# Performance work log

Measured on AMD Instinct MI355X. Metric: run time of the kernel, lower is better.

Reference implementation:

```python
import jax, jax.numpy as jnp
import numpy as np

D = 256; NH = 8; NL = 4; NP = 4; HD = D // NH
SHAPES = np.array([[180, 180], [90, 90], [45, 45], [23, 23]], dtype=np.int32)
LQ = int((SHAPES[:, 0] * SHAPES[:, 1]).sum())  # 43054
STARTS = np.concatenate([[0], np.cumsum(SHAPES[:, 0] * SHAPES[:, 1])[:-1]]).astype(np.int32)


def setup_inputs():
    ks = jax.random.split(jax.random.key(0), 16)
    s = 0.02
    p = lambda k, shp: jax.random.normal(k, shp, jnp.float32) * s
    return {
        "query": jax.random.normal(ks[0], (1, LQ, D), jnp.float32),
        "ref_points": jax.random.uniform(ks[1], (1, LQ, NL, 2), dtype=jnp.float32),
        "pos": jax.random.normal(ks[2], (1, LQ, D), jnp.float32),
        "input_spatial_shapes": jnp.asarray(SHAPES),
        "input_level_start_index": jnp.asarray(STARTS),
        "w_off": p(ks[3], (D, NH * NL * NP * 2)), "b_off": p(ks[4], (NH * NL * NP * 2,)),
        "w_attn": p(ks[5], (D, NH * NL * NP)), "b_attn": p(ks[6], (NH * NL * NP,)),
        "w_val": p(ks[7], (D, D)), "b_val": jnp.zeros((D,), jnp.float32),
        "w_out": p(ks[8], (D, D)), "b_out": jnp.zeros((D,), jnp.float32),
        "g1": jnp.ones((D,), jnp.float32), "beta1": jnp.zeros((D,), jnp.float32),
        "w1": p(ks[9], (D, D)), "b1": jnp.zeros((D,), jnp.float32),
        "w2": p(ks[10], (D, D)), "b2": jnp.zeros((D,), jnp.float32),
        "g2": jnp.ones((D,), jnp.float32), "beta2": jnp.zeros((D,), jnp.float32),
    }


def _ln(x, g, b):
    m = x.mean(-1, keepdims=True)
    v = ((x - m) ** 2).mean(-1, keepdims=True)
    return (x - m) * jax.lax.rsqrt(v + 1e-5) * g + b


def _sample_level(v, Hl, Wl, loc):
    # v: (B, Hl*Wl, NH, HD); loc: (B, Lq, NH, NP, 2) normalized to [0,1]
    # Bilinear sampling matching F.grid_sample(align_corners=False, padding_mode='zeros')
    B, _, nh, d = v.shape
    Lq, P = loc.shape[1], loc.shape[3]
    vb = jnp.transpose(v, (0, 2, 1, 3))  # (B, NH, HW, d)
    x = loc[..., 0] * Wl - 0.5
    y = loc[..., 1] * Hl - 0.5
    x0 = jnp.floor(x); y0 = jnp.floor(y)
    fx = x - x0; fy = y - y0
    out = jnp.zeros((B, nh, Lq, P, d), v.dtype)
    for dy in (0, 1):
        for dx in (0, 1):
            xi = x0 + dx; yi = y0 + dy
            w = (fx if dx else 1.0 - fx) * (fy if dy else 1.0 - fy)
            valid = (xi >= 0) & (xi < Wl) & (yi >= 0) & (yi < Hl)
            xc = jnp.clip(xi, 0, Wl - 1).astype(jnp.int32)
            yc = jnp.clip(yi, 0, Hl - 1).astype(jnp.int32)
            idx = jnp.transpose(yc * Wl + xc, (0, 2, 1, 3)).reshape(B, nh, Lq * P)
            g = jnp.take_along_axis(vb, idx[..., None], axis=2).reshape(B, nh, Lq, P, d)
            wt = jnp.transpose(jnp.where(valid, w, 0.0), (0, 2, 1, 3))
            out = out + g * wt[..., None]
    return out  # (B, NH, Lq, NP, HD)


def _layer(query, ref_points, pos, shp, sti, w_off, b_off, w_attn, b_attn, w_val, b_val,
           w_out, b_out, g1, beta1, w1, b1, w2, b2, g2, beta2):
    B, Lq, _ = query.shape
    q = query + pos  # with_pos_embed
    value = (query @ w_val + b_val).reshape(B, Lq, NH, HD)
    off = (q @ w_off + b_off).reshape(B, Lq, NH, NL, NP, 2)
    aw = jax.nn.softmax((q @ w_attn + b_attn).reshape(B, Lq, NH, NL * NP), axis=-1)
    aw = aw.reshape(B, Lq, NH, NL, NP)
    # offset_normalizer = [W_l, H_l]
    norm = jnp.asarray(shp[:, ::-1].copy(), jnp.float32)
    loc = ref_points[:, :, None, :, None, :] + off / norm[None, None, None, :, None, :]
    acc = jnp.zeros((B, NH, Lq, HD), query.dtype)
    for l in range(NL):
        Hl, Wl = int(shp[l, 0]), int(shp[l, 1])
        st = int(sti[l])
        sampled = _sample_level(value[:, st:st + Hl * Wl], Hl, Wl, loc[:, :, :, l])
        wl = jnp.transpose(aw[:, :, :, l], (0, 2, 1, 3))  # (B, NH, Lq, NP)
        acc = acc + (sampled * wl[..., None]).sum(axis=3)
    attn_out = acc.transpose(0, 2, 1, 3).reshape(B, Lq, D) @ w_out + b_out
    # residual + LayerNorm + FFN (dropout is identity in eval mode)
    x = _ln(query + attn_out, g1, beta1)
    ffn = jax.nn.relu(x @ w1 + b1) @ w2 + b2
    return _ln(x + ffn, g2, beta2)


def reference(query, ref_points, pos, input_spatial_shapes, input_level_start_index,
              w_off, b_off, w_attn, b_attn, w_val, b_val, w_out, b_out,
              g1, beta1, w1, b1, w2, b2, g2, beta2):
    shp = np.asarray(input_spatial_shapes)
    sti = np.asarray(input_level_start_index)
    return _layer(query, ref_points, pos, shp, sti, w_off, b_off, w_attn, b_attn,
                  w_val, b_val, w_out, b_out, g1, beta1, w1, b1, w2, b2, g2, beta2)
```

## Files before the change

kernel.cpp:

```cpp
#include <hip/hip_runtime.h>

typedef unsigned short u16;
typedef unsigned int u32;
typedef float f32x4 __attribute__((ext_vector_type(4)));
typedef short i16x8 __attribute__((ext_vector_type(8)));
typedef __bf16 bf16x8_t __attribute__((ext_vector_type(8)));

#define LQ 43054

__device__ __forceinline__ float bf2f(u16 u) {
  union { u32 i; float f; } v; v.i = ((u32)u) << 16; return v.f;
}
__device__ __forceinline__ u16 f2bf(float f) {
  u32 i = __float_as_uint(f);
  return (u16)((i + 0x7FFFu + ((i >> 16) & 1u)) >> 16);
}

__device__ __forceinline__ float dot2bf(u32 v, u32 w, float c) {
  float d;
  asm("v_dot2_f32_bf16 %0, %1, %2, %3" : "=v"(d) : "v"(v), "v"(w), "v"(c));
  return d;
}

template <typename T>
__device__ __forceinline__ auto mfma_try(T a, T b, f32x4 c, int)
    -> decltype(__builtin_amdgcn_mfma_f32_16x16x32_bf16(a, b, c, 0, 0, 0)) {
  return __builtin_amdgcn_mfma_f32_16x16x32_bf16(a, b, c, 0, 0, 0);
}
template <typename T>
__device__ __forceinline__ f32x4 mfma_try(T a, T b, f32x4 c, long) {
  return __builtin_amdgcn_mfma_f32_16x16x32_bf16(
      __builtin_bit_cast(bf16x8_t, a), __builtin_bit_cast(bf16x8_t, b), c, 0, 0, 0);
}
__device__ __forceinline__ f32x4 mfma_bf16(i16x8 a, i16x8 b, f32x4 c) {
  return mfma_try(a, b, c, 0);
}

__global__ void transpose_all_kernel(
    const float* __restrict__ w_off, const float* __restrict__ w_attn,
    const float* __restrict__ w_val, const float* __restrict__ w_out,
    const float* __restrict__ w1, const float* __restrict__ w2,
    u16* __restrict__ wT) {
  int b = blockIdx.x;
  const float* src; u16* dst; int N; int col;
  if (b < 256)       { src = w_off;  dst = wT;          N = 256; col = b; }
  else if (b < 384)  { src = w_attn; dst = wT + 65536;  N = 128; col = b - 256; }
  else if (b < 640)  { src = w_val;  dst = wT + 98304;  N = 256; col = b - 384; }
  else if (b < 896)  { src = w_out;  dst = wT + 163840; N = 256; col = b - 640; }
  else if (b < 1152) { src = w1;     dst = wT + 229376; N = 256; col = b - 896; }
  else               { src = w2;     dst = wT + 294912; N = 256; col = b - 1152; }
  dst[col * 256 + threadIdx.x] = f2bf(src[threadIdx.x * N + col]);
}

__device__ __forceinline__ void stage_a_dma(uint4* As, const u16* A, int r0, int M,
                                            int w, int lane) {
#pragma unroll
  for (int jj = 0; jj < 8; ++jj) {
    int row = w * 16 + jj * 2 + (lane >> 5);
    int gr = min(r0 + row, M - 1);
    int c = lane & 31;
    const uint4* gp = (const uint4*)A + (size_t)gr * 32 + (c ^ (row & 7));
    __builtin_amdgcn_global_load_lds(
        (const __attribute__((address_space(1))) void*)gp,
        (__attribute__((address_space(3))) void*)(As + (w * 16 + jj * 2) * 32),
        16, 0, 0);
  }
}
template <int ADD, int PH>
__device__ __forceinline__ void stage_a_f32(uint4* As, const float* A, const float* A2,
                                            int r0, int M, int tid) {
  constexpr int IT = 16 / PH;
#pragma unroll
  for (int h = 0; h < PH; ++h) {
    float4 va[IT];
    float4 vp[ADD ? IT : 1];
#pragma unroll
    for (int it = 0; it < IT; ++it) {
      int e = tid + (h * IT + it) * 256;
      int gr = min(r0 + (e >> 6), M - 1);
      int idx = gr * 64 + (e & 63);
      va[it] = ((const float4*)A)[idx];
      if constexpr (ADD) vp[it] = ((const float4*)A2)[idx];
    }
#pragma unroll
    for (int it = 0; it < IT; ++it) {
      int e = tid + (h * IT + it) * 256;
      int row = e >> 6, c4 = e & 63;
      float4 v = va[it];
      if constexpr (ADD) {
        v.x += vp[it].x; v.y += vp[it].y; v.z += vp[it].z; v.w += vp[it].w;
      }
      uint2 pk;
      pk.x = (u32)f2bf(v.x) | ((u32)f2bf(v.y) << 16);
      pk.y = (u32)f2bf(v.z) | ((u32)f2bf(v.w) << 16);
      int c = c4 >> 1, hf = c4 & 1;
      ((uint2*)As)[((row * 32 + (c ^ (row & 7))) << 1) | hf] = pk;
    }
  }
}
__device__ __forceinline__ void load_b(i16x8* f, const u16* Bt, int t, int l16, int quad) {
  const uint4* bp = (const uint4*)Bt + (t * 16 + l16) * 32 + quad;
#pragma unroll
  for (int kk = 0; kk < 8; ++kk) f[kk] = __builtin_bit_cast(i16x8, bp[kk << 2]);
}
__device__ __forceinline__ void tile_mfma(f32x4* acc, const uint4* As,
                                          const i16x8* bfr, int l16, int quad) {
#pragma unroll
  for (int rg = 0; rg < 4; ++rg) {
    int arow = rg * 16 + l16;
    f32x4 a = {0.f, 0.f, 0.f, 0.f};
#pragma unroll
    for (int kk = 0; kk < 8; ++kk) {
      i16x8 afr = __builtin_bit_cast(i16x8, As[arow * 32 + (((kk << 2) + quad) ^ (arow & 7))]);
      a = mfma_bf16(afr, bfr[kk], a);
    }
    acc[rg] = a;
  }
}

__device__ __forceinline__ int swz_u16(int row, int col) {
  return row * 256 + ((((col >> 3) ^ (row & 7)) << 3) | (col & 7));
}

#define LS_STRIDE 264
__device__ __forceinline__ void lds_store_rows(const u16* Ls, u16* out,
                                               int r0, int M, int w, int lane) {
#pragma unroll
  for (int it = 0; it < 8; ++it) {
    int lrow = w * 16 + it * 2 + (lane >> 5);
    int grow = r0 + lrow;
    int chunk = lane & 31;
    if (grow < M) {
      *(uint4*)(out + (size_t)grow * 256 + chunk * 8) =
          *(const uint4*)(Ls + lrow * LS_STRIDE + chunk * 8);
    }
  }
}

template <int AIN, int MODE>
__global__ __launch_bounds__(256, 3) void gemm_kernel(
    const void* __restrict__ Av, const u16* __restrict__ Bt,
    const float* __restrict__ bias, void* __restrict__ out, int M) {
  __shared__ uint4 As[2176];
  const int tid = threadIdx.x;
  const int w = tid >> 6, lane = tid & 63, quad = lane >> 4, l16 = lane & 15;
  const int r0 = blockIdx.x * 64;
  if constexpr (AIN == 2) stage_a_dma(As, (const u16*)Av, r0, M, w, lane);
  else                    stage_a_f32<0, 2>(As, (const float*)Av, nullptr, r0, M, tid);
  __syncthreads();
  i16x8 bfr[2][8];
  load_b(bfr[0], Bt, w * 4, l16, quad);
  f32x4 vals[4][4];
#pragma unroll
  for (int i = 0; i < 4; ++i) {
    const int t = w * 4 + i;
    if (i + 1 < 4) load_b(bfr[(i + 1) & 1], Bt, t + 1, l16, quad);
    tile_mfma(vals[i], As, bfr[i & 1], l16, quad);
  }
  __syncthreads();
  u16* Ls = (u16*)As;
#pragma unroll
  for (int i = 0; i < 4; ++i) {
    const int col = (w * 4 + i) * 16 + l16;
    const float bv = bias[col];
#pragma unroll
    for (int rg = 0; rg < 4; ++rg)
#pragma unroll
      for (int r = 0; r < 4; ++r) {
        float v = vals[i][rg][r] + bv;
        if (MODE == 2) v = fmaxf(v, 0.f);
        Ls[(rg * 16 + (quad << 2) + r) * LS_STRIDE + col] = f2bf(v);
      }
  }
  __syncthreads();
  lds_store_rows(Ls, (u16*)out, r0, M, w, lane);
}

__global__ __launch_bounds__(256, 3) void offaw_gemm_kernel(
    const float* __restrict__ query, const float* __restrict__ pos,
    const u16* __restrict__ Bt, const float* __restrict__ b_off,
    const float* __restrict__ b_attn, u16* __restrict__ offb,
    float* __restrict__ aw, int M) {
  __shared__ uint4 As[2176];
  const int tid = threadIdx.x;
  const int w = tid >> 6, lane = tid & 63, quad = lane >> 4, l16 = lane & 15;
  const int r0 = blockIdx.x * 64;
  stage_a_f32<1, 4>(As, query, pos, r0, M, tid);
  __syncthreads();
  i16x8 bfr[2][8];
  load_b(bfr[0], Bt, w, l16, quad);
  f32x4 vals[4][4];
#pragma unroll
  for (int i = 0; i < 6; ++i) {
    const int t = w + 4 * i;
    if (i + 1 < 6) load_b(bfr[(i + 1) & 1], Bt, w + 4 * (i + 1), l16, quad);
    if (i < 4) {
      tile_mfma(vals[i], As, bfr[i & 1], l16, quad);
    } else {
      f32x4 acc[4];
      tile_mfma(acc, As, bfr[i & 1], l16, quad);
      const int colc = (t - 16) * 16 + l16;
      const float bv = b_attn[colc];
#pragma unroll
      for (int rg = 0; rg < 4; ++rg)
#pragma unroll
        for (int r = 0; r < 4; ++r) {
          float v = acc[rg][r] + bv;
          float m = v;
#pragma unroll
          for (int o = 1; o < 16; o <<= 1) m = fmaxf(m, __shfl_xor(m, o));
          float e = __expf(v - m);
          float s = e;
#pragma unroll
          for (int o = 1; o < 16; o <<= 1) s += __shfl_xor(s, o);
          int row = r0 + rg * 16 + (quad << 2) + r;
          if (row < M) aw[row * 128 + colc] = e / s;
        }
    }
  }
  __syncthreads();
  u16* Ls = (u16*)As;
#pragma unroll
  for (int i = 0; i < 4; ++i) {
    const int col = (w + 4 * i) * 16 + l16;
    const float bv = b_off[col];
#pragma unroll
    for (int rg = 0; rg < 4; ++rg)
#pragma unroll
      for (int r = 0; r < 4; ++r)
        Ls[(rg * 16 + (quad << 2) + r) * LS_STRIDE + col] = f2bf(vals[i][rg][r] + bv);
  }
  __syncthreads();
  lds_store_rows(Ls, offb, r0, M, w, lane);
}

__global__ __launch_bounds__(256, 2) void tail_fused_kernel(
    const u16* __restrict__ accb, const u16* __restrict__ woutT,
    const float* __restrict__ b_out, const float* __restrict__ query,
    const float* __restrict__ g1, const float* __restrict__ beta1,
    const u16* __restrict__ w1T, const float* __restrict__ b1,
    const u16* __restrict__ w2T, const float* __restrict__ b2,
    const float* __restrict__ g2, const float* __restrict__ beta2,
    float* __restrict__ out, int M) {
  __shared__ uint4 As[2048];
  __shared__ uint4 Xs[2048];
  __shared__ float2 pnorm[256];
  const int tid = threadIdx.x;
  const int w = tid >> 6, lane = tid & 63, quad = lane >> 4, l16 = lane & 15;
  const int r0 = blockIdx.x * 64;
  stage_a_dma(As, accb, r0, M, w, lane);
  __syncthreads();
  i16x8 bfr[2][8];
  f32x4 vals[4][4];
  float s[16], s2[16];

  load_b(bfr[0], woutT, w * 4, l16, quad);
#pragma unroll
  for (int i = 0; i < 4; ++i) {
    if (i + 1 < 4) load_b(bfr[(i + 1) & 1], woutT, w * 4 + i + 1, l16, quad);
    tile_mfma(vals[i], As, bfr[i & 1], l16, quad);
  }
#pragma unroll
  for (int k = 0; k < 16; ++k) { s[k] = 0.f; s2[k] = 0.f; }
#pragma unroll
  for (int i = 0; i < 4; ++i) {
    const int col = (w * 4 + i) * 16 + l16;
    const float bv = b_out[col];
#pragma unroll
    for (int rg = 0; rg < 4; ++rg)
#pragma unroll
      for (int r = 0; r < 4; ++r) {
        int row = r0 + rg * 16 + (quad << 2) + r;
        float rv = (row < M) ? query[row * 256 + col] : 0.f;
        float v = vals[i][rg][r] + bv + rv;
        vals[i][rg][r] = v;
        s[rg * 4 + r] += v; s2[rg * 4 + r] += v * v;
      }
  }
#pragma unroll
  for (int k = 0; k < 16; ++k)
#pragma unroll
    for (int o = 1; o < 16; o <<= 1) {
      s[k] += __shfl_xor(s[k], o);
      s2[k] += __shfl_xor(s2[k], o);
    }
  if (l16 == 0) {
#pragma unroll
    for (int rg = 0; rg < 4; ++rg)
#pragma unroll
      for (int r = 0; r < 4; ++r)
        pnorm[(rg * 16 + (quad << 2) + r) * 4 + w] = make_float2(s[rg * 4 + r], s2[rg * 4 + r]);
  }
  __syncthreads();
  u16* Xu = (u16*)Xs;
#pragma unroll
  for (int rg = 0; rg < 4; ++rg)
#pragma unroll
    for (int r = 0; r < 4; ++r) {
      int lrow = rg * 16 + (quad << 2) + r;
      float4 p01 = ((const float4*)pnorm)[lrow * 2];
      float4 p23 = ((const float4*)pnorm)[lrow * 2 + 1];
      float ss = p01.x + p01.z + p23.x + p23.z;
      float qq = p01.y + p01.w + p23.y + p23.w;
      float mean = ss * (1.f / 256.f);
      float var = qq * (1.f / 256.f) - mean * mean;
      float inv = rsqrtf(var + 1e-5f);
#pragma unroll
      for (int i = 0; i < 4; ++i) {
        const int col = (w * 4 + i) * 16 + l16;
        float o = (vals[i][rg][r] - mean) * inv * g1[col] + beta1[col];
        Xu[swz_u16(lrow, col)] = f2bf(o);
      }
    }
  __syncthreads();

  load_b(bfr[0], w1T, w * 4, l16, quad);
#pragma unroll
  for (int i = 0; i < 4; ++i) {
    if (i + 1 < 4) load_b(bfr[(i + 1) & 1], w1T, w * 4 + i + 1, l16, quad);
    tile_mfma(vals[i], Xs, bfr[i & 1], l16, quad);
  }
  u16* Hu = (u16*)As;
#pragma unroll
  for (int i = 0; i < 4; ++i) {
    const int col = (w * 4 + i) * 16 + l16;
    const float bv = b1[col];
#pragma unroll
    for (int rg = 0; rg < 4; ++rg)
#pragma unroll
      for (int r = 0; r < 4; ++r) {
        int lrow = rg * 16 + (quad << 2) + r;
        Hu[swz_u16(lrow, col)] = f2bf(fmaxf(vals[i][rg][r] + bv, 0.f));
      }
  }
  __syncthreads();

  load_b(bfr[0], w2T, w * 4, l16, quad);
#pragma unroll
  for (int i = 0; i < 4; ++i) {
    if (i + 1 < 4) load_b(bfr[(i + 1) & 1], w2T, w * 4 + i + 1, l16, quad);
    tile_mfma(vals[i], As, bfr[i & 1], l16, quad);
  }
#pragma unroll
  for (int k = 0; k < 16; ++k) { s[k] = 0.f; s2[k] = 0.f; }
#pragma unroll
  for (int i = 0; i < 4; ++i) {
    const int col = (w * 4 + i) * 16 + l16;
    const float bv = b2[col];
#pragma unroll
    for (int rg = 0; rg < 4; ++rg)
#pragma unroll
      for (int r = 0; r < 4; ++r) {
        int lrow = rg * 16 + (quad << 2) + r;
        float xv = bf2f(Xu[swz_u16(lrow, col)]);
        float v = vals[i][rg][r] + bv + xv;
        vals[i][rg][r] = v;
        s[rg * 4 + r] += v; s2[rg * 4 + r] += v * v;
      }
  }
#pragma unroll
  for (int k = 0; k < 16; ++k)
#pragma unroll
    for (int o = 1; o < 16; o <<= 1) {
      s[k] += __shfl_xor(s[k], o);
      s2[k] += __shfl_xor(s2[k], o);
    }
  if (l16 == 0) {
#pragma unroll
    for (int rg = 0; rg < 4; ++rg)
#pragma unroll
      for (int r = 0; r < 4; ++r)
        pnorm[(rg * 16 + (quad << 2) + r) * 4 + w] = make_float2(s[rg * 4 + r], s2[rg * 4 + r]);
  }
  __syncthreads();
#pragma unroll
  for (int rg = 0; rg < 4; ++rg)
#pragma unroll
    for (int r = 0; r < 4; ++r) {
      int lrow = rg * 16 + (quad << 2) + r;
      float4 p01 = ((const float4*)pnorm)[lrow * 2];
      float4 p23 = ((const float4*)pnorm)[lrow * 2 + 1];
      float ss = p01.x + p01.z + p23.x + p23.z;
      float qq = p01.y + p01.w + p23.y + p23.w;
      float mean = ss * (1.f / 256.f);
      float var = qq * (1.f / 256.f) - mean * mean;
      float inv = rsqrtf(var + 1e-5f);
      int row = r0 + lrow;
      if (row < M) {
#pragma unroll
        for (int i = 0; i < 4; ++i) {
          const int col = (w * 4 + i) * 16 + l16;
          out[row * 256 + col] = (vals[i][rg][r] - mean) * inv * g2[col] + beta2[col];
        }
      }
    }
}

__global__ __launch_bounds__(256) void sampler_kernel(
    const float* __restrict__ refp, const u16* __restrict__ offb,
    const float* __restrict__ aw, const u16* __restrict__ value,
    u32* __restrict__ accv) {
  __shared__ uint4 rec[544];
  const int t = threadIdx.x;
  const int nwg = gridDim.x;
  const int qd = nwg >> 3, rm = nwg & 7;
  const int xcd = blockIdx.x & 7, ii = blockIdx.x >> 3;
  const int b = (xcd < rm ? xcd * (qd + 1) : rm * (qd + 1) + (xcd - rm) * qd) + ii;
#pragma unroll
  for (int it = 0; it < 2; ++it) {
    const int sidx = t + it * 256;
    const int qs = sidx >> 7, j = sidx & 127;
    const int i = b * 4 + qs;
    if (i < LQ) {
      const int h = j >> 4, lp = j & 15, l = lp >> 2;
      const int Wl = (l == 0) ? 180 : (l == 1) ? 90 : (l == 2) ? 45 : 23;
      const int st = (l == 0) ? 0 : (l == 1) ? 32400 : (l == 2) ? 40500 : 42525;
      const float wj = aw[i * 128 + j];
      const u32 o2 = *(const u32*)(offb + i * 256 + h * 32 + lp * 2);
      const float ox = bf2f((u16)(o2 & 0xffffu)), oy = bf2f((u16)(o2 >> 16));
      const float rx = refp[i * 8 + l * 2], ry = refp[i * 8 + l * 2 + 1];
      float x = rx * (float)Wl + ox - 0.5f;
      float y = ry * (float)Wl + oy - 0.5f;
      float x0f = floorf(x), y0f = floorf(y);
      float fx = x - x0f, fy = y - y0f;
      int x0 = (int)x0f, y0 = (int)y0f;
      bool vx0 = (x0 >= 0) & (x0 < Wl), vx1 = (x0 + 1 >= 0) & (x0 + 1 < Wl);
      bool vy0 = (y0 >= 0) & (y0 < Wl), vy1 = (y0 + 1 >= 0) & (y0 + 1 < Wl);
      int x0c = min(max(x0, 0), Wl - 1), x1c = min(max(x0 + 1, 0), Wl - 1);
      int y0c = min(max(y0, 0), Wl - 1), y1c = min(max(y0 + 1, 0), Wl - 1);
      float w00 = (vx0 & vy0) ? wj * (1.f - fx) * (1.f - fy) : 0.f;
      float w01 = (vx1 & vy0) ? wj * fx * (1.f - fy) : 0.f;
      float w10 = (vx0 & vy1) ? wj * (1.f - fx) * fy : 0.f;
      float w11 = (vx1 & vy1) ? wj * fx * fy : 0.f;
      uint4 r;
      r.x = (u32)((st + y0c * Wl + x0c) * 512 + h * 64) | (u32)(x1c - x0c);
      r.y = (u32)(y1c - y0c) * (u32)(Wl * 512);
      r.z = (u32)f2bf(w00) | ((u32)f2bf(w01) << 16);
      r.w = (u32)f2bf(w10) | ((u32)f2bf(w11) << 16);
      rec[qs * 136 + h * 17 + lp] = r;
    }
  }
  __syncthreads();
  const int qs = t >> 6, j2 = t & 63;
  const int h = j2 >> 3, dp8 = j2 & 7;
  const int i = b * 4 + qs;
  if (i >= LQ) return;
  const char* vb = (const char*)value;
  float a0 = 0.f, a1 = 0.f, a2 = 0.f, a3 = 0.f;
  const int rbase = qs * 136 + h * 17;
  const u32 dpo = (u32)(dp8 * 8);
#pragma unroll
  for (int p = 0; p < 16; ++p) {
    uint4 r = rec[rbase + p];
    u32 base = (r.x & 0xFFFFFFFEu) + dpo;
    u32 dxo = (r.x & 1u) << 9;
    u32 dyo = r.y;
    uint2 p00 = *(const uint2*)(vb + base);
    uint2 p01 = *(const uint2*)(vb + base + dxo);
    uint2 p10 = *(const uint2*)(vb + base + dyo);
    uint2 p11 = *(const uint2*)(vb + base + dyo + dxo);
    a0 = dot2bf(__builtin_amdgcn_perm(p01.x, p00.x, 0x05040100u), r.z, a0);
    a1 = dot2bf(__builtin_amdgcn_perm(p01.x, p00.x, 0x07060302u), r.z, a1);
    a2 = dot2bf(__builtin_amdgcn_perm(p01.y, p00.y, 0x05040100u), r.z, a2);
    a3 = dot2bf(__builtin_amdgcn_perm(p01.y, p00.y, 0x07060302u), r.z, a3);
    a0 = dot2bf(__builtin_amdgcn_perm(p11.x, p10.x, 0x05040100u), r.w, a0);
    a1 = dot2bf(__builtin_amdgcn_perm(p11.x, p10.x, 0x07060302u), r.w, a1);
    a2 = dot2bf(__builtin_amdgcn_perm(p11.y, p10.y, 0x05040100u), r.w, a2);
    a3 = dot2bf(__builtin_amdgcn_perm(p11.y, p10.y, 0x07060302u), r.w, a3);
  }
  uint2 pk;
  pk.x = (u32)f2bf(a0) | ((u32)f2bf(a1) << 16);
  pk.y = (u32)f2bf(a2) | ((u32)f2bf(a3) << 16);
  ((uint2*)accv)[i * 64 + h * 8 + dp8] = pk;
}

extern "C" void kernel_launch(void* const* d_in, const int* in_sizes, int n_in,
                              void* d_out, int out_size, void* d_ws, size_t ws_size,
                              hipStream_t stream) {
  const float* query  = (const float*)d_in[0];
  const float* refp   = (const float*)d_in[1];
  const float* pos    = (const float*)d_in[2];
  const float* w_off  = (const float*)d_in[5];
  const float* b_off  = (const float*)d_in[6];
  const float* w_attn = (const float*)d_in[7];
  const float* b_attn = (const float*)d_in[8];
  const float* w_val  = (const float*)d_in[9];
  const float* b_val  = (const float*)d_in[10];
  const float* w_out  = (const float*)d_in[11];
  const float* b_out  = (const float*)d_in[12];
  const float* g1     = (const float*)d_in[13];
  const float* beta1  = (const float*)d_in[14];
  const float* w1     = (const float*)d_in[15];
  const float* b1     = (const float*)d_in[16];
  const float* w2     = (const float*)d_in[17];
  const float* b2     = (const float*)d_in[18];
  const float* g2     = (const float*)d_in[19];
  const float* beta2  = (const float*)d_in[20];

  char* ws = (char*)d_ws;
  u16*   wT    = (u16*)(ws + 0);
  u16*   value = (u16*)(ws + 720896);
  u16*   offb  = (u16*)(ws + 22764544);
  float* aw    = (float*)(ws + 44808192);
  u16*   accb  = (u16*)(ws + 66851840);

  u16* woffT  = wT;
  u16* wvalT  = wT + 98304;
  u16* woutT  = wT + 163840;
  u16* w1T    = wT + 229376;
  u16* w2T    = wT + 294912;

  transpose_all_kernel<<<1408, 256, 0, stream>>>(w_off, w_attn, w_val, w_out, w1, w2, wT);

  const int gm = (LQ + 63) / 64;
  gemm_kernel<0, 1><<<gm, 256, 0, stream>>>(query, wvalT, b_val, value, LQ);
  offaw_gemm_kernel<<<gm, 256, 0, stream>>>(query, pos, woffT, b_off, b_attn, offb, aw, LQ);
  const int sb = (LQ + 3) / 4;
  sampler_kernel<<<sb, 256, 0, stream>>>(refp, offb, aw, value, (u32*)accb);
  tail_fused_kernel<<<gm, 256, 0, stream>>>(accb, woutT, b_out, query, g1, beta1,
                                            w1T, b1, w2T, b2, g2, beta2,
                                            (float*)d_out, LQ);
}
```

Baseline: 407.5 us.

## Halve tail kernel row tile to 32 and raise occupancy, stage output stores

The fused tail kernel (out-proj, LN, FFN, LN) now processes 32 rows per block instead of 64, with half the LDS and accumulator registers, and launch bounds raised to 4 blocks per SM. A-tile staging is done inline with global_load_lds, and the B-fragment double buffering is dropped. The final LayerNorm output is staged through LDS so each row is written with coalesced float4 stores. This trades more blocks and repeated weight-fragment loads for higher occupancy and better store coalescing.

After: 394.4 us. -3.2%, faster.

```diff
diff --git a/kernel.cpp b/kernel.cpp
--- a/kernel.cpp
+++ b/kernel.cpp
@@ -117,6 +117,20 @@
     acc[rg] = a;
   }
 }
+__device__ __forceinline__ void tile_mfma2(f32x4* acc, const uint4* As,
+                                           const i16x8* bfr, int l16, int quad) {
+#pragma unroll
+  for (int rg = 0; rg < 2; ++rg) {
+    int arow = rg * 16 + l16;
+    f32x4 a = {0.f, 0.f, 0.f, 0.f};
+#pragma unroll
+    for (int kk = 0; kk < 8; ++kk) {
+      i16x8 afr = __builtin_bit_cast(i16x8, As[arow * 32 + (((kk << 2) + quad) ^ (arow & 7))]);
+      a = mfma_bf16(afr, bfr[kk], a);
+    }
+    acc[rg] = a;
+  }
+}
 
 __device__ __forceinline__ int swz_u16(int row, int col) {
   return row * 256 + ((((col >> 3) ^ (row & 7)) << 3) | (col & 7));
@@ -234,7 +248,7 @@
   lds_store_rows(Ls, offb, r0, M, w, lane);
 }
 
-__global__ __launch_bounds__(256, 2) void tail_fused_kernel(
+__global__ __launch_bounds__(256, 4) void tail_fused_kernel(
     const u16* __restrict__ accb, const u16* __restrict__ woutT,
     const float* __restrict__ b_out, const float* __restrict__ query,
     const float* __restrict__ g1, const float* __restrict__ beta1,
@@ -242,32 +256,42 @@
     const u16* __restrict__ w2T, const float* __restrict__ b2,
     const float* __restrict__ g2, const float* __restrict__ beta2,
     float* __restrict__ out, int M) {
-  __shared__ uint4 As[2048];
-  __shared__ uint4 Xs[2048];
-  __shared__ float2 pnorm[256];
+  __shared__ uint4 smem[2112];
+  uint4* As = smem;
+  uint4* Xs = smem + 1024;
+  float2* pnorm = (float2*)(smem + 2048);
   const int tid = threadIdx.x;
   const int w = tid >> 6, lane = tid & 63, quad = lane >> 4, l16 = lane & 15;
-  const int r0 = blockIdx.x * 64;
-  stage_a_dma(As, accb, r0, M, w, lane);
-  __syncthreads();
-  i16x8 bfr[2][8];
-  f32x4 vals[4][4];
-  float s[16], s2[16];
-
-  load_b(bfr[0], woutT, w * 4, l16, quad);
-#pragma unroll
-  for (int i = 0; i < 4; ++i) {
-    if (i + 1 < 4) load_b(bfr[(i + 1) & 1], woutT, w * 4 + i + 1, l16, quad);
-    tile_mfma(vals[i], As, bfr[i & 1], l16, quad);
-  }
-#pragma unroll
-  for (int k = 0; k < 16; ++k) { s[k] = 0.f; s2[k] = 0.f; }
+  const int r0 = blockIdx.x * 32;
+#pragma unroll
+  for (int jj = 0; jj < 4; ++jj) {
+    int row = w * 8 + jj * 2 + (lane >> 5);
+    int gr = min(r0 + row, M - 1);
+    int c = lane & 31;
+    const uint4* gp = (const uint4*)accb + (size_t)gr * 32 + (c ^ (row & 7));
+    __builtin_amdgcn_global_load_lds(
+        (const __attribute__((address_space(1))) void*)gp,
+        (__attribute__((address_space(3))) void*)(As + (w * 8 + jj * 2) * 32),
+        16, 0, 0);
+  }
+  __syncthreads();
+  i16x8 bfr[8];
+  f32x4 vals[4][2];
+  float s[8], s2[8];
+
+#pragma unroll
+  for (int i = 0; i < 4; ++i) {
+    load_b(bfr, woutT, w * 4 + i, l16, quad);
+    tile_mfma2(vals[i], As, bfr, l16, quad);
+  }
+#pragma unroll
+  for (int k = 0; k < 8; ++k) { s[k] = 0.f; s2[k] = 0.f; }
 #pragma unroll
   for (int i = 0; i < 4; ++i) {
     const int col = (w * 4 + i) * 16 + l16;
     const float bv = b_out[col];
 #pragma unroll
-    for (int rg = 0; rg < 4; ++rg)
+    for (int rg = 0; rg < 2; ++rg)
 #pragma unroll
       for (int r = 0; r < 4; ++r) {
         int row = r0 + rg * 16 + (quad << 2) + r;
@@ -278,7 +302,7 @@
       }
   }
 #pragma unroll
-  for (int k = 0; k < 16; ++k)
+  for (int k = 0; k < 8; ++k)
 #pragma unroll
     for (int o = 1; o < 16; o <<= 1) {
       s[k] += __shfl_xor(s[k], o);
@@ -286,7 +310,7 @@
     }
   if (l16 == 0) {
 #pragma unroll
-    for (int rg = 0; rg < 4; ++rg)
+    for (int rg = 0; rg < 2; ++rg)
 #pragma unroll
       for (int r = 0; r < 4; ++r)
         pnorm[(rg * 16 + (quad << 2) + r) * 4 + w] = make_float2(s[rg * 4 + r], s2[rg * 4 + r]);
@@ -294,7 +318,7 @@
   __syncthreads();
   u16* Xu = (u16*)Xs;
 #pragma unroll
-  for (int rg = 0; rg < 4; ++rg)
+  for (int rg = 0; rg < 2; ++rg)
 #pragma unroll
     for (int r = 0; r < 4; ++r) {
       int lrow = rg * 16 + (quad << 2) + r;
@@ -314,11 +338,10 @@
     }
   __syncthreads();
 
-  load_b(bfr[0], w1T, w * 4, l16, quad);
-#pragma unroll
-  for (int i = 0; i < 4; ++i) {
-    if (i + 1 < 4) load_b(bfr[(i + 1) & 1], w1T, w * 4 + i + 1, l16, quad);
-    tile_mfma(vals[i], Xs, bfr[i & 1], l16, quad);
+#pragma unroll
+  for (int i = 0; i < 4; ++i) {
+    load_b(bfr, w1T, w * 4 + i, l16, quad);
+    tile_mfma2(vals[i], Xs, bfr, l16, quad);
   }
   u16* Hu = (u16*)As;
 #pragma unroll
@@ -326,7 +349,7 @@
     const int col = (w * 4 + i) * 16 + l16;
     const float bv = b1[col];
 #pragma unroll
-    for (int rg = 0; rg < 4; ++rg)
+    for (int rg = 0; rg < 2; ++rg)
 #pragma unroll
       for (int r = 0; r < 4; ++r) {
         int lrow = rg * 16 + (quad << 2) + r;
@@ -335,20 +358,19 @@
   }
   __syncthreads();
 
-  load_b(bfr[0], w2T, w * 4, l16, quad);
-#pragma unroll
-  for (int i = 0; i < 4; ++i) {
-    if (i + 1 < 4) load_b(bfr[(i + 1) & 1], w2T, w * 4 + i + 1, l16, quad);
-    tile_mfma(vals[i], As, bfr[i & 1], l16, quad);
-  }
-#pragma unroll
-  for (int k = 0; k < 16; ++k) { s[k] = 0.f; s2[k] = 0.f; }
+#pragma unroll
+  for (int i = 0; i < 4; ++i) {
+    load_b(bfr, w2T, w * 4 + i, l16, quad);
+    tile_mfma2(vals[i], As, bfr, l16, quad);
+  }
+#pragma unroll
+  for (int k = 0; k < 8; ++k) { s[k] = 0.f; s2[k] = 0.f; }
 #pragma unroll
   for (int i = 0; i < 4; ++i) {
     const int col = (w * 4 + i) * 16 + l16;
     const float bv = b2[col];
 #pragma unroll
-    for (int rg = 0; rg < 4; ++rg)
+    for (int rg = 0; rg < 2; ++rg)
 #pragma unroll
       for (int r = 0; r < 4; ++r) {
         int lrow = rg * 16 + (quad << 2) + r;
@@ -359,7 +381,7 @@
       }
   }
 #pragma unroll
-  for (int k = 0; k < 16; ++k)
+  for (int k = 0; k < 8; ++k)
 #pragma unroll
     for (int o = 1; o < 16; o <<= 1) {
       s[k] += __shfl_xor(s[k], o);
@@ -367,14 +389,15 @@
     }
   if (l16 == 0) {
 #pragma unroll
-    for (int rg = 0; rg < 4; ++rg)
+    for (int rg = 0; rg < 2; ++rg)
 #pragma unroll
       for (int r = 0; r < 4; ++r)
         pnorm[(rg * 16 + (quad << 2) + r) * 4 + w] = make_float2(s[rg * 4 + r], s2[rg * 4 + r]);
   }
   __syncthreads();
-#pragma unroll
-  for (int rg = 0; rg < 4; ++rg)
+  float* stg = (float*)smem;
+#pragma unroll
+  for (int rg = 0; rg < 2; ++rg) {
 #pragma unroll
     for (int r = 0; r < 4; ++r) {
       int lrow = rg * 16 + (quad << 2) + r;
@@ -385,15 +408,23 @@
       float mean = ss * (1.f / 256.f);
       float var = qq * (1.f / 256.f) - mean * mean;
       float inv = rsqrtf(var + 1e-5f);
-      int row = r0 + lrow;
-      if (row < M) {
-#pragma unroll
-        for (int i = 0; i < 4; ++i) {
-          const int col = (w * 4 + i) * 16 + l16;
-          out[row * 256 + col] = (vals[i][rg][r] - mean) * inv * g2[col] + beta2[col];
-        }
-      }
-    }
+#pragma unroll
+      for (int i = 0; i < 4; ++i) {
+        const int col = (w * 4 + i) * 16 + l16;
+        stg[((quad << 2) + r) * 268 + col] = (vals[i][rg][r] - mean) * inv * g2[col] + beta2[col];
+      }
+    }
+    __syncthreads();
+#pragma unroll
+    for (int rr = 0; rr < 4; ++rr) {
+      int lr = w * 4 + rr;
+      int grow = r0 + rg * 16 + lr;
+      if (grow < M)
+        *(float4*)(out + (size_t)grow * 256 + lane * 4) =
+            *(const float4*)(stg + lr * 268 + lane * 4);
+    }
+    if (rg == 0) __syncthreads();
+  }
 }
 
 __global__ __launch_bounds__(256) void sampler_kernel(
@@ -517,7 +548,8 @@
   offaw_gemm_kernel<<<gm, 256, 0, stream>>>(query, pos, woffT, b_off, b_attn, offb, aw, LQ);
   const int sb = (LQ + 3) / 4;
   sampler_kernel<<<sb, 256, 0, stream>>>(refp, offb, aw, value, (u32*)accb);
-  tail_fused_kernel<<<gm, 256, 0, stream>>>(accb, woutT, b_out, query, g1, beta1,
+  const int gt = (LQ + 31) / 32;
+  tail_fused_kernel<<<gt, 256, 0, stream>>>(accb, woutT, b_out, query, g1, beta1,
                                             w1T, b1, w2T, b2, g2, beta2,
                                             (float*)d_out, LQ);
 }
```
